# Kernel optimization log

Measured on AMD Instinct MI355X. Metric: run time of the kernel, lower is better.

Reference implementation:

```python
import jax, jax.numpy as jnp
import numpy as np

B, U, D = 128, 200, 512

def setup_inputs() -> dict:
    key = jax.random.key(0)
    k1, k2, k3 = jax.random.split(key, 3)
    input_real = jax.random.normal(k1, (B, D, D), dtype=jnp.float32)
    input_imag = jax.random.normal(k2, (B, D, D), dtype=jnp.float32)
    # keras 'uniform' initializer: U(-0.05, 0.05); unit_norm constraint normalizes over axes (1,2)
    kernel = jax.random.uniform(k3, (U, D, 2), dtype=jnp.float32, minval=-0.05, maxval=0.05)
    kernel = kernel / jnp.linalg.norm(kernel.reshape(U, -1), axis=1)[:, None, None]
    return {"input_real": input_real, "input_imag": input_imag, "kernel": kernel}

def reference(input_real, input_imag, kernel):
    # kernel: [U, D, 2] -> real/imag measurement vectors
    kr = kernel[:, :, 0]  # [U, D]
    ki = kernel[:, :, 1]  # [U, D]
    # Original: M_real = kr kr^T - ki ki^T ; M_imag = ki kr^T + kr ki^T (outer products per unit)
    # out[b,n] = trace(R_b @ M_real_n) - trace(I_b @ M_imag_n)
    # trace(A @ (u v^T)) = sum_ij A[i,j] u[j] v[i] -> quadratic form, avoids [B,U,D,D] tiles.
    t_real = (jnp.einsum('bij,nj,ni->bn', input_real, kr, kr)
              - jnp.einsum('bij,nj,ni->bn', input_real, ki, ki))
    t_imag = (jnp.einsum('bij,nj,ni->bn', input_imag, ki, kr)
              + jnp.einsum('bij,nj,ni->bn', input_imag, kr, ki))
    return t_real - t_imag  # [B, U]
```

## Files before the change

kernel.cpp:

```cpp
#include <hip/hip_runtime.h>
#include <hip/hip_bf16.h>
#include <string.h>

#define BB 128
#define UU 200
#define DD 512
#define NP 256

typedef __attribute__((ext_vector_type(8))) short short8;
typedef __attribute__((ext_vector_type(4))) float f32x4;

__device__ __forceinline__ unsigned pack_bf16_2(float a, float b) {
    __hip_bfloat162 h = __float22bfloat162_rn(make_float2(a, b));
    unsigned u; memcpy(&u, &h, 4); return u;
}

__device__ __forceinline__ unsigned short f2bf(float x) {
    union { float f; unsigned u; } v; v.f = x;
    unsigned r = v.u + 0x7FFFu + ((v.u >> 16) & 1u);
    return (unsigned short)(r >> 16);
}

__global__ void kb2_build_kernel(const float* __restrict__ Kt,
                                 unsigned short* __restrict__ Kbr,
                                 unsigned short* __restrict__ Kbi,
                                 float* __restrict__ out) {
    int idx = blockIdx.x * 256 + threadIdx.x;
    int n = idx >> 9, j = idx & 511;
    unsigned short r = 0, im = 0;
    if (n < UU) {
        float2 s = ((const float2*)Kt)[(size_t)n * DD + j];
        r = f2bf(s.x); im = f2bf(s.y);
    }
    Kbr[idx] = r;
    Kbi[idx] = im;
    if (idx < BB * UU) out[idx] = 0.0f;
}

__global__ void zero_out_kernel(float* __restrict__ out) {
    int i = blockIdx.x * 256 + threadIdx.x;
    if (i < BB * UU) out[i] = 0.0f;
}

__global__ __launch_bounds__(512, 4) void qf_gemm_kernel(
    const float* __restrict__ Ar, const float* __restrict__ Ai,
    const float* __restrict__ Kt,
    const unsigned short* __restrict__ Kbr, const unsigned short* __restrict__ Kbi,
    float* __restrict__ out)
{
    __shared__ short sA[2][2][32 * 64];

    const int tid  = threadIdx.x;
    const int bx   = blockIdx.x;
    const int b    = bx >> 4;
    const int i0   = (bx & 15) * 32;

    const int w    = tid >> 6;
    const int lane = tid & 63;
    const int rrow = lane & 15;
    const int quad = lane >> 4;
    const int xr   = rrow & 7;
    const int nn0  = w * 32 + rrow;
    const int nn1  = nn0 + 16;

    const int g  = tid & 15;
    const int r0 = tid >> 4;
    const float* ArB = Ar + ((size_t)b * DD + i0) * DD;
    const float* AiB = Ai + ((size_t)b * DD + i0) * DD;
    const unsigned aoff  = (unsigned)r0 * DD + (unsigned)g * 4;
    const int      waddr = r0 * 64 + (((g >> 1) ^ (r0 & 7)) * 8) + (g & 1) * 4;

    const int rb0 = rrow * 64 + ((quad ^ xr)) * 8;
    const int rb1 = rrow * 64 + ((quad ^ xr) ^ 4) * 8;

    f32x4 accr[2][2], acci[2][2];
#pragma unroll
    for (int m = 0; m < 2; ++m)
#pragma unroll
        for (int nt = 0; nt < 2; ++nt) { accr[m][nt] = (f32x4)(0.f); acci[m][nt] = (f32x4)(0.f); }

    f32x4 pf[2];
    pf[0] = *(const f32x4*)(ArB + aoff);
    pf[1] = *(const f32x4*)(AiB + aoff);

#pragma unroll 2
    for (int ss = 0; ss < 8; ++ss) {
        short* bufR = &sA[ss & 1][0][0];
        short* bufI = &sA[ss & 1][1][0];

        {
            uint2 u, v;
            u.x = pack_bf16_2(pf[0][0], pf[0][1]);
            u.y = pack_bf16_2(pf[0][2], pf[0][3]);
            v.x = pack_bf16_2(pf[1][0], pf[1][1]);
            v.y = pack_bf16_2(pf[1][2], pf[1][3]);
            *(uint2*)&bufR[waddr] = u;
            *(uint2*)&bufI[waddr] = v;
        }
        __syncthreads();

        if (ss < 7) {
            const unsigned jn = (unsigned)(ss + 1) * 64;
            pf[0] = *(const f32x4*)(ArB + aoff + jn);
            pf[1] = *(const f32x4*)(AiB + aoff + jn);
        }

        const int jbase = ss * 64;
#pragma unroll
        for (int kk = 0; kk < 2; ++kk) {
            const int j = jbase + kk * 32 + quad * 8;
            short8 bkr0 = *(const short8*)(Kbr + (size_t)nn0 * 512 + j);
            short8 bkr1 = *(const short8*)(Kbr + (size_t)nn1 * 512 + j);
            short8 bki0 = *(const short8*)(Kbi + (size_t)nn0 * 512 + j);
            short8 bki1 = *(const short8*)(Kbi + (size_t)nn1 * 512 + j);
            const int rb = kk ? rb1 : rb0;

            short8 afR[2];
#pragma unroll
            for (int m = 0; m < 2; ++m)
                afR[m] = *(const short8*)&bufR[rb + m * 1024];
#pragma unroll
            for (int m = 0; m < 2; ++m) {
                accr[m][0] = __builtin_amdgcn_mfma_f32_16x16x32_bf16(afR[m], bkr0, accr[m][0], 0, 0, 0);
                accr[m][1] = __builtin_amdgcn_mfma_f32_16x16x32_bf16(afR[m], bkr1, accr[m][1], 0, 0, 0);
                acci[m][0] = __builtin_amdgcn_mfma_f32_16x16x32_bf16(afR[m], bki0, acci[m][0], 0, 0, 0);
                acci[m][1] = __builtin_amdgcn_mfma_f32_16x16x32_bf16(afR[m], bki1, acci[m][1], 0, 0, 0);
            }

            union { short8 v; unsigned u[4]; } t0, t1;
            t0.v = bki0; t1.v = bki1;
#pragma unroll
            for (int e = 0; e < 4; ++e) { t0.u[e] ^= 0x80008000u; t1.u[e] ^= 0x80008000u; }

            short8 afI[2];
#pragma unroll
            for (int m = 0; m < 2; ++m)
                afI[m] = *(const short8*)&bufI[rb + m * 1024];
#pragma unroll
            for (int m = 0; m < 2; ++m) {
                accr[m][0] = __builtin_amdgcn_mfma_f32_16x16x32_bf16(afI[m], t0.v, accr[m][0], 0, 0, 0);
                accr[m][1] = __builtin_amdgcn_mfma_f32_16x16x32_bf16(afI[m], t1.v, accr[m][1], 0, 0, 0);
                acci[m][0] = __builtin_amdgcn_mfma_f32_16x16x32_bf16(afI[m], bkr0, acci[m][0], 0, 0, 0);
                acci[m][1] = __builtin_amdgcn_mfma_f32_16x16x32_bf16(afI[m], bkr1, acci[m][1], 0, 0, 0);
            }
        }
    }

    float* outB = out + (size_t)b * UU;
#pragma unroll
    for (int nt = 0; nt < 2; ++nt) {
        const int n = w * 32 + nt * 16 + rrow;
        float s = 0.f;
        if (n < UU) {
            const float* kp = Kt + ((size_t)n * DD + i0 + quad * 4) * 2;
#pragma unroll
            for (int m = 0; m < 2; ++m) {
                f32x4 k01 = *(const f32x4*)(kp + m * 32);
                f32x4 k23 = *(const f32x4*)(kp + m * 32 + 4);
                s += accr[m][nt][0] * k01[0] - acci[m][nt][0] * k01[1];
                s += accr[m][nt][1] * k01[2] - acci[m][nt][1] * k01[3];
                s += accr[m][nt][2] * k23[0] - acci[m][nt][2] * k23[1];
                s += accr[m][nt][3] * k23[2] - acci[m][nt][3] * k23[3];
            }
        }
        s += __shfl_xor(s, 16, 64);
        s += __shfl_xor(s, 32, 64);
        if (quad == 0 && n < UU)
            atomicAdd(&outB[n], s);
    }
}

#define ASTR 40
#define WSTR 40
__global__ __launch_bounds__(512, 4) void cm_gemm_fb_kernel(
    const float* __restrict__ Ar, const float* __restrict__ Ai,
    const float* __restrict__ Kt, float* __restrict__ dst)
{
    __shared__ short sAr[BB * ASTR];
    __shared__ short sAi[BB * ASTR];
    __shared__ short sWr[NP * WSTR];
    __shared__ short sWi[NP * WSTR];
    const int tid = threadIdx.x, irow = blockIdx.x;
    const int w = tid >> 6, lane = tid & 63;
    const int mw = (w & 1) * 64, nw = (w >> 1) * 64;
    const int rrow = lane & 15, quad = lane >> 4;
    const int nW = tid >> 1, jh = (tid & 1) * 16;
    float krI = 0.f, kiI = 0.f;
    if (nW < UU) { float2 s = ((const float2*)Kt)[(size_t)nW * DD + irow]; krI = s.x; kiI = s.y; }
    const int brow0 = tid >> 3, grp = tid & 7;
    const size_t aoff0 = (size_t)brow0 * DD * DD + (size_t)irow * DD + (size_t)grp * 4;
    const size_t aoff1 = aoff0 + (size_t)64 * DD * DD;
    f32x4 acc[4][4];
#pragma unroll
    for (int a = 0; a < 4; ++a)
#pragma unroll
        for (int c = 0; c < 4; ++c) acc[a][c] = (f32x4)(0.f);
    for (int jw = 0; jw < DD; jw += 32) {
        f32x4 vr0 = *(const f32x4*)(Ar + aoff0 + jw);
        f32x4 vr1 = *(const f32x4*)(Ar + aoff1 + jw);
        f32x4 vi0 = *(const f32x4*)(Ai + aoff0 + jw);
        f32x4 vi1 = *(const f32x4*)(Ai + aoff1 + jw);
        union { unsigned short s[4]; uint2 u; } t0, t1, t2, t3;
#pragma unroll
        for (int q = 0; q < 4; ++q) {
            t0.s[q] = f2bf(vr0[q]); t1.s[q] = f2bf(vr1[q]);
            t2.s[q] = f2bf(vi0[q]); t3.s[q] = f2bf(vi1[q]);
        }
        *(uint2*)&sAr[ brow0       * ASTR + grp * 4] = t0.u;
        *(uint2*)&sAr[(brow0 + 64) * ASTR + grp * 4] = t1.u;
        *(uint2*)&sAi[ brow0       * ASTR + grp * 4] = t2.u;
        *(uint2*)&sAi[(brow0 + 64) * ASTR + grp * 4] = t3.u;
        if (nW < UU) {
            const f32x4* kv = (const f32x4*)(Kt + (size_t)nW * DD * 2 + (size_t)(jw + jh) * 2);
#pragma unroll
            for (int q = 0; q < 8; ++q) {
                f32x4 v = kv[q];
                float wr0 = krI * v[0] - kiI * v[1], wi0 = -(krI * v[1] + kiI * v[0]);
                float wr1 = krI * v[2] - kiI * v[3], wi1 = -(krI * v[3] + kiI * v[2]);
                *(unsigned*)&sWr[nW * WSTR + jh + 2 * q] = (unsigned)f2bf(wr0) | ((unsigned)f2bf(wr1) << 16);
                *(unsigned*)&sWi[nW * WSTR + jh + 2 * q] = (unsigned)f2bf(wi0) | ((unsigned)f2bf(wi1) << 16);
            }
        } else {
#pragma unroll
            for (int q = 0; q < 8; ++q) {
                *(unsigned*)&sWr[nW * WSTR + jh + 2 * q] = 0u;
                *(unsigned*)&sWi[nW * WSTR + jh + 2 * q] = 0u;
            }
        }
        __syncthreads();
#pragma unroll
        for (int ph = 0; ph < 2; ++ph) {
            const short* sA = ph ? sAi : sAr;
            const short* sW = ph ? sWi : sWr;
            short8 af[4], bf[4];
#pragma unroll
            for (int t = 0; t < 4; ++t) {
                af[t] = *(const short8*)&sA[(mw + t * 16 + rrow) * ASTR + quad * 8];
                bf[t] = *(const short8*)&sW[(nw + t * 16 + rrow) * WSTR + quad * 8];
            }
#pragma unroll
            for (int ti = 0; ti < 4; ++ti)
#pragma unroll
                for (int tj = 0; tj < 4; ++tj)
                    acc[ti][tj] = __builtin_amdgcn_mfma_f32_16x16x32_bf16(af[ti], bf[tj], acc[ti][tj], 0, 0, 0);
        }
        __syncthreads();
    }
#pragma unroll
    for (int ti = 0; ti < 4; ++ti) {
        int m = mw + ti * 16 + quad * 4;
#pragma unroll
        for (int tj = 0; tj < 4; ++tj) {
            int n = nw + tj * 16 + rrow;
            if (n < UU)
#pragma unroll
                for (int r = 0; r < 4; ++r)
                    atomicAdd(&dst[(size_t)(m + r) * UU + n], acc[ti][tj][r]);
        }
    }
}

extern "C" void kernel_launch(void* const* d_in, const int* in_sizes, int n_in,
                              void* d_out, int out_size, void* d_ws, size_t ws_size,
                              hipStream_t stream) {
    const float* Ar = (const float*)d_in[0];
    const float* Ai = (const float*)d_in[1];
    const float* Kt = (const float*)d_in[2];
    float* out = (float*)d_out;

    const size_t kb_need = (size_t)2 * NP * DD * sizeof(unsigned short);

    if (ws_size >= kb_need) {
        unsigned short* Kbr = (unsigned short*)d_ws;
        unsigned short* Kbi = Kbr + (size_t)NP * DD;
        hipLaunchKernelGGL(kb2_build_kernel, dim3(512), dim3(256), 0, stream, Kt, Kbr, Kbi, out);
        hipLaunchKernelGGL(qf_gemm_kernel, dim3(2048), dim3(512), 0, stream,
                           Ar, Ai, Kt, Kbr, Kbi, out);
    } else {
        hipLaunchKernelGGL(zero_out_kernel, dim3(100), dim3(256), 0, stream, out);
        hipLaunchKernelGGL(cm_gemm_fb_kernel, dim3(DD), dim3(512), 0, stream, Ar, Ai, Kt, out);
    }
}
```

Before: 355.9 us.

## Use 1024-thread blocks with 64-row A tiles and two-stage-ahead prefetch

Each block now covers 64 rows of the input matrix instead of 32 and runs 16 waves, each owning 16 measurement units rather than 32. This halves the per-wave B-fragment loads relative to MFMA work, and doubles the reuse of each staged A tile across units. The global prefetch of A now runs two stages ahead through two alternating register sets. Costs are fewer blocks (1024), a larger per-block barrier, doubled LDS use, and possible register pressure at the 1024-thread launch bound.

After: 314.7 us. 1.13x faster.

```diff
diff --git a/kernel.cpp b/kernel.cpp
--- a/kernel.cpp
+++ b/kernel.cpp
@@ -42,26 +42,25 @@
     if (i < BB * UU) out[i] = 0.0f;
 }
 
-__global__ __launch_bounds__(512, 4) void qf_gemm_kernel(
+__global__ __launch_bounds__(1024, 4) void qf_gemm_kernel(
     const float* __restrict__ Ar, const float* __restrict__ Ai,
     const float* __restrict__ Kt,
     const unsigned short* __restrict__ Kbr, const unsigned short* __restrict__ Kbi,
     float* __restrict__ out)
 {
-    __shared__ short sA[2][2][32 * 64];
+    __shared__ short sA[2][2][64 * 64];
 
     const int tid  = threadIdx.x;
     const int bx   = blockIdx.x;
-    const int b    = bx >> 4;
-    const int i0   = (bx & 15) * 32;
+    const int b    = bx >> 3;
+    const int i0   = (bx & 7) * 64;
 
     const int w    = tid >> 6;
     const int lane = tid & 63;
     const int rrow = lane & 15;
     const int quad = lane >> 4;
     const int xr   = rrow & 7;
-    const int nn0  = w * 32 + rrow;
-    const int nn1  = nn0 + 16;
+    const int nn   = w * 16 + rrow;
 
     const int g  = tid & 15;
     const int r0 = tid >> 4;
@@ -73,94 +72,95 @@
     const int rb0 = rrow * 64 + ((quad ^ xr)) * 8;
     const int rb1 = rrow * 64 + ((quad ^ xr) ^ 4) * 8;
 
-    f32x4 accr[2][2], acci[2][2];
-#pragma unroll
-    for (int m = 0; m < 2; ++m)
-#pragma unroll
-        for (int nt = 0; nt < 2; ++nt) { accr[m][nt] = (f32x4)(0.f); acci[m][nt] = (f32x4)(0.f); }
-
-    f32x4 pf[2];
-    pf[0] = *(const f32x4*)(ArB + aoff);
-    pf[1] = *(const f32x4*)(AiB + aoff);
-
-#pragma unroll 2
-    for (int ss = 0; ss < 8; ++ss) {
-        short* bufR = &sA[ss & 1][0][0];
-        short* bufI = &sA[ss & 1][1][0];
-
-        {
-            uint2 u, v;
-            u.x = pack_bf16_2(pf[0][0], pf[0][1]);
-            u.y = pack_bf16_2(pf[0][2], pf[0][3]);
-            v.x = pack_bf16_2(pf[1][0], pf[1][1]);
-            v.y = pack_bf16_2(pf[1][2], pf[1][3]);
-            *(uint2*)&bufR[waddr] = u;
-            *(uint2*)&bufI[waddr] = v;
-        }
-        __syncthreads();
-
-        if (ss < 7) {
-            const unsigned jn = (unsigned)(ss + 1) * 64;
-            pf[0] = *(const f32x4*)(ArB + aoff + jn);
-            pf[1] = *(const f32x4*)(AiB + aoff + jn);
-        }
-
-        const int jbase = ss * 64;
-#pragma unroll
-        for (int kk = 0; kk < 2; ++kk) {
-            const int j = jbase + kk * 32 + quad * 8;
-            short8 bkr0 = *(const short8*)(Kbr + (size_t)nn0 * 512 + j);
-            short8 bkr1 = *(const short8*)(Kbr + (size_t)nn1 * 512 + j);
-            short8 bki0 = *(const short8*)(Kbi + (size_t)nn0 * 512 + j);
-            short8 bki1 = *(const short8*)(Kbi + (size_t)nn1 * 512 + j);
-            const int rb = kk ? rb1 : rb0;
-
-            short8 afR[2];
-#pragma unroll
-            for (int m = 0; m < 2; ++m)
-                afR[m] = *(const short8*)&bufR[rb + m * 1024];
-#pragma unroll
-            for (int m = 0; m < 2; ++m) {
-                accr[m][0] = __builtin_amdgcn_mfma_f32_16x16x32_bf16(afR[m], bkr0, accr[m][0], 0, 0, 0);
-                accr[m][1] = __builtin_amdgcn_mfma_f32_16x16x32_bf16(afR[m], bkr1, accr[m][1], 0, 0, 0);
-                acci[m][0] = __builtin_amdgcn_mfma_f32_16x16x32_bf16(afR[m], bki0, acci[m][0], 0, 0, 0);
-                acci[m][1] = __builtin_amdgcn_mfma_f32_16x16x32_bf16(afR[m], bki1, acci[m][1], 0, 0, 0);
-            }
-
-            union { short8 v; unsigned u[4]; } t0, t1;
-            t0.v = bki0; t1.v = bki1;
-#pragma unroll
-            for (int e = 0; e < 4; ++e) { t0.u[e] ^= 0x80008000u; t1.u[e] ^= 0x80008000u; }
-
-            short8 afI[2];
-#pragma unroll
-            for (int m = 0; m < 2; ++m)
-                afI[m] = *(const short8*)&bufI[rb + m * 1024];
-#pragma unroll
-            for (int m = 0; m < 2; ++m) {
-                accr[m][0] = __builtin_amdgcn_mfma_f32_16x16x32_bf16(afI[m], t0.v, accr[m][0], 0, 0, 0);
-                accr[m][1] = __builtin_amdgcn_mfma_f32_16x16x32_bf16(afI[m], t1.v, accr[m][1], 0, 0, 0);
-                acci[m][0] = __builtin_amdgcn_mfma_f32_16x16x32_bf16(afI[m], bkr0, acci[m][0], 0, 0, 0);
-                acci[m][1] = __builtin_amdgcn_mfma_f32_16x16x32_bf16(afI[m], bkr1, acci[m][1], 0, 0, 0);
-            }
-        }
-    }
+    const unsigned short* kbrp = Kbr + (size_t)nn * 512;
+    const unsigned short* kbip = Kbi + (size_t)nn * 512;
+
+    f32x4 accr[4], acci[4];
+#pragma unroll
+    for (int m = 0; m < 4; ++m) { accr[m] = (f32x4)(0.f); acci[m] = (f32x4)(0.f); }
+
+    f32x4 pfA[2], pfB[2];
+    pfA[0] = *(const f32x4*)(ArB + aoff);
+    pfA[1] = *(const f32x4*)(AiB + aoff);
+    pfB[0] = *(const f32x4*)(ArB + aoff + 64);
+    pfB[1] = *(const f32x4*)(AiB + aoff + 64);
+
+#define QF_SUBSTAGE(SS, PF)                                                     \
+    {                                                                           \
+        const int ss = (SS);                                                    \
+        short* bufR = &sA[ss & 1][0][0];                                        \
+        short* bufI = &sA[ss & 1][1][0];                                        \
+        uint2 u, v;                                                             \
+        u.x = pack_bf16_2(PF[0][0], PF[0][1]);                                  \
+        u.y = pack_bf16_2(PF[0][2], PF[0][3]);                                  \
+        v.x = pack_bf16_2(PF[1][0], PF[1][1]);                                  \
+        v.y = pack_bf16_2(PF[1][2], PF[1][3]);                                  \
+        *(uint2*)&bufR[waddr] = u;                                              \
+        *(uint2*)&bufI[waddr] = v;                                              \
+        __syncthreads();                                                        \
+         \
+        const int jb = ss * 64 + quad * 8;                                      \
+        short8 bkr0 = *(const short8*)(kbrp + jb);                              \
+        short8 bki0 = *(const short8*)(kbip + jb);                              \
+        short8 bkr1 = *(const short8*)(kbrp + jb + 32);                         \
+        short8 bki1 = *(const short8*)(kbip + jb + 32);                         \
+           \
+        if (ss < 6) {                                                           \
+            const unsigned jn = aoff + (unsigned)(ss + 2) * 64;                 \
+            PF[0] = *(const f32x4*)(ArB + jn);                                  \
+            PF[1] = *(const f32x4*)(AiB + jn);                                  \
+        }                                                                       \
+        _Pragma("unroll")                                                       \
+        for (int kk = 0; kk < 2; ++kk) {                                        \
+            const short8 bkr = kk ? bkr1 : bkr0;                                \
+            const short8 bki = kk ? bki1 : bki0;                                \
+            const int rb = kk ? rb1 : rb0;                                      \
+            short8 afR[4];                                                      \
+            _Pragma("unroll")                                                   \
+            for (int m = 0; m < 4; ++m)                                         \
+                afR[m] = *(const short8*)&bufR[rb + m * 1024];                  \
+            _Pragma("unroll")                                                   \
+            for (int m = 0; m < 4; ++m) {                                       \
+                accr[m] = __builtin_amdgcn_mfma_f32_16x16x32_bf16(afR[m], bkr, accr[m], 0, 0, 0); \
+                acci[m] = __builtin_amdgcn_mfma_f32_16x16x32_bf16(afR[m], bki, acci[m], 0, 0, 0); \
+            }                                                                   \
+            union { short8 sv; unsigned uu[4]; } nb;                            \
+            nb.sv = bki;                                                        \
+            _Pragma("unroll")                                                   \
+            for (int e = 0; e < 4; ++e) nb.uu[e] ^= 0x80008000u;                \
+            short8 afI[4];                                                      \
+            _Pragma("unroll")                                                   \
+            for (int m = 0; m < 4; ++m)                                         \
+                afI[m] = *(const short8*)&bufI[rb + m * 1024];                  \
+            _Pragma("unroll")                                                   \
+            for (int m = 0; m < 4; ++m) {                                       \
+                accr[m] = __builtin_amdgcn_mfma_f32_16x16x32_bf16(afI[m], nb.sv, accr[m], 0, 0, 0); \
+                acci[m] = __builtin_amdgcn_mfma_f32_16x16x32_bf16(afI[m], bkr, acci[m], 0, 0, 0);   \
+            }                                                                   \
+        }                                                                       \
+    }
+
+#pragma unroll
+    for (int sp = 0; sp < 4; ++sp) {
+        QF_SUBSTAGE(2 * sp,     pfA)
+        QF_SUBSTAGE(2 * sp + 1, pfB)
+    }
+#undef QF_SUBSTAGE
 
     float* outB = out + (size_t)b * UU;
-#pragma unroll
-    for (int nt = 0; nt < 2; ++nt) {
-        const int n = w * 32 + nt * 16 + rrow;
+    {
+        const int n = nn;
         float s = 0.f;
         if (n < UU) {
             const float* kp = Kt + ((size_t)n * DD + i0 + quad * 4) * 2;
 #pragma unroll
-            for (int m = 0; m < 2; ++m) {
+            for (int m = 0; m < 4; ++m) {
                 f32x4 k01 = *(const f32x4*)(kp + m * 32);
                 f32x4 k23 = *(const f32x4*)(kp + m * 32 + 4);
-                s += accr[m][nt][0] * k01[0] - acci[m][nt][0] * k01[1];
-                s += accr[m][nt][1] * k01[2] - acci[m][nt][1] * k01[3];
-                s += accr[m][nt][2] * k23[0] - acci[m][nt][2] * k23[1];
-                s += accr[m][nt][3] * k23[2] - acci[m][nt][3] * k23[3];
+                s += accr[m][0] * k01[0] - acci[m][0] * k01[1];
+                s += accr[m][1] * k01[2] - acci[m][1] * k01[3];
+                s += accr[m][2] * k23[0] - acci[m][2] * k23[1];
+                s += accr[m][3] * k23[2] - acci[m][3] * k23[3];
             }
         }
         s += __shfl_xor(s, 16, 64);
@@ -274,7 +274,7 @@
         unsigned short* Kbr = (unsigned short*)d_ws;
         unsigned short* Kbi = Kbr + (size_t)NP * DD;
         hipLaunchKernelGGL(kb2_build_kernel, dim3(512), dim3(256), 0, stream, Kt, Kbr, Kbi, out);
-        hipLaunchKernelGGL(qf_gemm_kernel, dim3(2048), dim3(512), 0, stream,
+        hipLaunchKernelGGL(qf_gemm_kernel, dim3(1024), dim3(1024), 0, stream,
                            Ar, Ai, Kt, Kbr, Kbi, out);
     } else {
         hipLaunchKernelGGL(zero_out_kernel, dim3(100), dim3(256), 0, stream, out);
```

## Stream fp32 A tiles to LDS via global_load_lds and use 32x32 MFMA

Applied to the files above, without the earlier changes.

The A-tile staging now uses direct global-to-LDS async loads of fp32 data, with XOR-swizzled addressing, instead of register prefetch plus bf16 packing before the LDS store. The bf16 conversion moves to after the LDS read. The MFMA shape changes from 16x16x32 to 32x32x16, and each warp covers 32 units, so warp 7 stays idle. This aims to cut register pressure and VGPR round-trips in the load path and to raise occupancy (launch bounds 4→5). In exchange it doubles LDS footprint, repeats the bf16 conversion per warp, and wastes one of the eight warps.

Result: slower. 378.6 us (+6.4%).

```diff
diff --git a/kernel.cpp b/kernel.cpp
--- a/kernel.cpp
+++ b/kernel.cpp
@@ -9,6 +9,7 @@
 
 typedef __attribute__((ext_vector_type(8))) short short8;
 typedef __attribute__((ext_vector_type(4))) float f32x4;
+typedef __attribute__((ext_vector_type(16))) float f32x16;
 
 __device__ __forceinline__ unsigned pack_bf16_2(float a, float b) {
     __hip_bfloat162 h = __float22bfloat162_rn(make_float2(a, b));
@@ -19,6 +20,12 @@
     union { float f; unsigned u; } v; v.f = x;
     unsigned r = v.u + 0x7FFFu + ((v.u >> 16) & 1u);
     return (unsigned short)(r >> 16);
+}
+
+__device__ __forceinline__ void glds16(const float* g, float* l) {
+    __builtin_amdgcn_global_load_lds(
+        (const __attribute__((address_space(1))) unsigned*)g,
+        (__attribute__((address_space(3))) unsigned*)l, 16, 0, 0);
 }
 
 __global__ void kb2_build_kernel(const float* __restrict__ Kt,
@@ -42,13 +49,13 @@
     if (i < BB * UU) out[i] = 0.0f;
 }
 
-__global__ __launch_bounds__(512, 4) void qf_gemm_kernel(
+__global__ __launch_bounds__(512, 5) void qf_gemm_kernel(
     const float* __restrict__ Ar, const float* __restrict__ Ai,
     const float* __restrict__ Kt,
     const unsigned short* __restrict__ Kbr, const unsigned short* __restrict__ Kbi,
     float* __restrict__ out)
 {
-    __shared__ short sA[2][2][32 * 64];
+    __shared__ float sAf[2][2][32 * 64];
 
     const int tid  = threadIdx.x;
     const int bx   = blockIdx.x;
@@ -57,116 +64,103 @@
 
     const int w    = tid >> 6;
     const int lane = tid & 63;
-    const int rrow = lane & 15;
-    const int quad = lane >> 4;
-    const int xr   = rrow & 7;
-    const int nn0  = w * 32 + rrow;
-    const int nn1  = nn0 + 16;
-
-    const int g  = tid & 15;
-    const int r0 = tid >> 4;
-    const float* ArB = Ar + ((size_t)b * DD + i0) * DD;
-    const float* AiB = Ai + ((size_t)b * DD + i0) * DD;
-    const unsigned aoff  = (unsigned)r0 * DD + (unsigned)g * 4;
-    const int      waddr = r0 * 64 + (((g >> 1) ^ (r0 & 7)) * 8) + (g & 1) * 4;
-
-    const int rb0 = rrow * 64 + ((quad ^ xr)) * 8;
-    const int rb1 = rrow * 64 + ((quad ^ xr) ^ 4) * 8;
-
-    f32x4 accr[2][2], acci[2][2];
-#pragma unroll
-    for (int m = 0; m < 2; ++m)
-#pragma unroll
-        for (int nt = 0; nt < 2; ++nt) { accr[m][nt] = (f32x4)(0.f); acci[m][nt] = (f32x4)(0.f); }
-
-    f32x4 pf[2];
-    pf[0] = *(const f32x4*)(ArB + aoff);
-    pf[1] = *(const f32x4*)(AiB + aoff);
+    const int l31  = lane & 31;
+    const int h    = lane >> 5;
+    const int key  = l31 & 15;
+
+    const int srow = w * 4 + (lane >> 4);
+    const int scol = (lane & 15) ^ (srow & 15);
+    const float* gR = Ar + ((size_t)b * DD + i0 + srow) * DD + scol * 4;
+    const float* gI = Ai + ((size_t)b * DD + i0 + srow) * DD + scol * 4;
+    const int ldsbase = w * 4 * 64;
+
+    const unsigned short* kbrp = Kbr + (size_t)(w * 32 + l31) * 512 + h * 8;
+    const unsigned short* kbip = Kbi + (size_t)(w * 32 + l31) * 512 + h * 8;
+
+    const int rb = l31 * 64;
+    int off0[4];
+#pragma unroll
+    for (int ks = 0; ks < 4; ++ks) {
+        int c0 = ks * 4 + 2 * h;
+        off0[ks] = rb + ((c0 ^ key) << 2);
+    }
+
+    f32x16 accr, acci;
+#pragma unroll
+    for (int e = 0; e < 16; ++e) { accr[e] = 0.f; acci[e] = 0.f; }
+
+    glds16(gR, &sAf[0][0][ldsbase]);
+    glds16(gI, &sAf[0][1][ldsbase]);
 
 #pragma unroll 2
     for (int ss = 0; ss < 8; ++ss) {
-        short* bufR = &sA[ss & 1][0][0];
-        short* bufI = &sA[ss & 1][1][0];
-
-        {
-            uint2 u, v;
-            u.x = pack_bf16_2(pf[0][0], pf[0][1]);
-            u.y = pack_bf16_2(pf[0][2], pf[0][3]);
-            v.x = pack_bf16_2(pf[1][0], pf[1][1]);
-            v.y = pack_bf16_2(pf[1][2], pf[1][3]);
-            *(uint2*)&bufR[waddr] = u;
-            *(uint2*)&bufI[waddr] = v;
-        }
         __syncthreads();
+        const float* bufR = &sAf[ss & 1][0][0];
+        const float* bufI = &sAf[ss & 1][1][0];
+
+        short8 kr[4], ki[4];
+        if (w < 7) {
+            const unsigned short* krp = kbrp + ss * 64;
+            const unsigned short* kip = kbip + ss * 64;
+#pragma unroll
+            for (int ks = 0; ks < 4; ++ks) {
+                kr[ks] = *(const short8*)(krp + ks * 16);
+                ki[ks] = *(const short8*)(kip + ks * 16);
+            }
+        }
+        __builtin_amdgcn_sched_barrier(0);
 
         if (ss < 7) {
-            const unsigned jn = (unsigned)(ss + 1) * 64;
-            pf[0] = *(const f32x4*)(ArB + aoff + jn);
-            pf[1] = *(const f32x4*)(AiB + aoff + jn);
-        }
-
-        const int jbase = ss * 64;
-#pragma unroll
-        for (int kk = 0; kk < 2; ++kk) {
-            const int j = jbase + kk * 32 + quad * 8;
-            short8 bkr0 = *(const short8*)(Kbr + (size_t)nn0 * 512 + j);
-            short8 bkr1 = *(const short8*)(Kbr + (size_t)nn1 * 512 + j);
-            short8 bki0 = *(const short8*)(Kbi + (size_t)nn0 * 512 + j);
-            short8 bki1 = *(const short8*)(Kbi + (size_t)nn1 * 512 + j);
-            const int rb = kk ? rb1 : rb0;
-
-            short8 afR[2];
-#pragma unroll
-            for (int m = 0; m < 2; ++m)
-                afR[m] = *(const short8*)&bufR[rb + m * 1024];
-#pragma unroll
-            for (int m = 0; m < 2; ++m) {
-                accr[m][0] = __builtin_amdgcn_mfma_f32_16x16x32_bf16(afR[m], bkr0, accr[m][0], 0, 0, 0);
-                accr[m][1] = __builtin_amdgcn_mfma_f32_16x16x32_bf16(afR[m], bkr1, accr[m][1], 0, 0, 0);
-                acci[m][0] = __builtin_amdgcn_mfma_f32_16x16x32_bf16(afR[m], bki0, acci[m][0], 0, 0, 0);
-                acci[m][1] = __builtin_amdgcn_mfma_f32_16x16x32_bf16(afR[m], bki1, acci[m][1], 0, 0, 0);
-            }
-
-            union { short8 v; unsigned u[4]; } t0, t1;
-            t0.v = bki0; t1.v = bki1;
-#pragma unroll
-            for (int e = 0; e < 4; ++e) { t0.u[e] ^= 0x80008000u; t1.u[e] ^= 0x80008000u; }
-
-            short8 afI[2];
-#pragma unroll
-            for (int m = 0; m < 2; ++m)
-                afI[m] = *(const short8*)&bufI[rb + m * 1024];
-#pragma unroll
-            for (int m = 0; m < 2; ++m) {
-                accr[m][0] = __builtin_amdgcn_mfma_f32_16x16x32_bf16(afI[m], t0.v, accr[m][0], 0, 0, 0);
-                accr[m][1] = __builtin_amdgcn_mfma_f32_16x16x32_bf16(afI[m], t1.v, accr[m][1], 0, 0, 0);
-                acci[m][0] = __builtin_amdgcn_mfma_f32_16x16x32_bf16(afI[m], bkr0, acci[m][0], 0, 0, 0);
-                acci[m][1] = __builtin_amdgcn_mfma_f32_16x16x32_bf16(afI[m], bkr1, acci[m][1], 0, 0, 0);
-            }
-        }
-    }
-
-    float* outB = out + (size_t)b * UU;
-#pragma unroll
-    for (int nt = 0; nt < 2; ++nt) {
-        const int n = w * 32 + nt * 16 + rrow;
+            glds16(gR + (ss + 1) * 64, &sAf[(ss + 1) & 1][0][ldsbase]);
+            glds16(gI + (ss + 1) * 64, &sAf[(ss + 1) & 1][1][ldsbase]);
+        }
+
+        if (w < 7) {
+#pragma unroll
+            for (int ks = 0; ks < 4; ++ks) {
+                const int o0 = off0[ks], o1 = off0[ks] ^ 4;
+                f32x4 a0 = *(const f32x4*)&bufR[o0];
+                f32x4 a1 = *(const f32x4*)&bufR[o1];
+                f32x4 b0 = *(const f32x4*)&bufI[o0];
+                f32x4 b1 = *(const f32x4*)&bufI[o1];
+                union { short8 v; unsigned u[4]; } fr, fi, nk;
+                fr.u[0] = pack_bf16_2(a0[0], a0[1]);
+                fr.u[1] = pack_bf16_2(a0[2], a0[3]);
+                fr.u[2] = pack_bf16_2(a1[0], a1[1]);
+                fr.u[3] = pack_bf16_2(a1[2], a1[3]);
+                fi.u[0] = pack_bf16_2(b0[0], b0[1]);
+                fi.u[1] = pack_bf16_2(b0[2], b0[3]);
+                fi.u[2] = pack_bf16_2(b1[0], b1[1]);
+                fi.u[3] = pack_bf16_2(b1[2], b1[3]);
+                nk.v = ki[ks];
+#pragma unroll
+                for (int e = 0; e < 4; ++e) nk.u[e] ^= 0x80008000u;
+                accr = __builtin_amdgcn_mfma_f32_32x32x16_bf16(fr.v, kr[ks], accr, 0, 0, 0);
+                acci = __builtin_amdgcn_mfma_f32_32x32x16_bf16(fr.v, ki[ks], acci, 0, 0, 0);
+                accr = __builtin_amdgcn_mfma_f32_32x32x16_bf16(fi.v, nk.v, accr, 0, 0, 0);
+                acci = __builtin_amdgcn_mfma_f32_32x32x16_bf16(fi.v, kr[ks], acci, 0, 0, 0);
+            }
+        }
+    }
+
+    if (w < 7) {
+        const int n = w * 32 + l31;
         float s = 0.f;
         if (n < UU) {
-            const float* kp = Kt + ((size_t)n * DD + i0 + quad * 4) * 2;
-#pragma unroll
-            for (int m = 0; m < 2; ++m) {
-                f32x4 k01 = *(const f32x4*)(kp + m * 32);
-                f32x4 k23 = *(const f32x4*)(kp + m * 32 + 4);
-                s += accr[m][nt][0] * k01[0] - acci[m][nt][0] * k01[1];
-                s += accr[m][nt][1] * k01[2] - acci[m][nt][1] * k01[3];
-                s += accr[m][nt][2] * k23[0] - acci[m][nt][2] * k23[1];
-                s += accr[m][nt][3] * k23[2] - acci[m][nt][3] * k23[3];
-            }
-        }
-        s += __shfl_xor(s, 16, 64);
+            const float* kp = Kt + ((size_t)n * DD + i0 + 4 * h) * 2;
+#pragma unroll
+            for (int q = 0; q < 4; ++q) {
+                f32x4 k01 = *(const f32x4*)(kp + q * 16);
+                f32x4 k23 = *(const f32x4*)(kp + q * 16 + 4);
+                s += accr[q * 4 + 0] * k01[0] - acci[q * 4 + 0] * k01[1];
+                s += accr[q * 4 + 1] * k01[2] - acci[q * 4 + 1] * k01[3];
+                s += accr[q * 4 + 2] * k23[0] - acci[q * 4 + 2] * k23[1];
+                s += accr[q * 4 + 3] * k23[2] - acci[q * 4 + 3] * k23[3];
+            }
+        }
         s += __shfl_xor(s, 32, 64);
-        if (quad == 0 && n < UU)
-            atomicAdd(&outB[n], s);
+        if (h == 0 && n < UU)
+            atomicAdd(&out[(size_t)b * UU + n], s);
     }
 }
 
```
